# Performance work log

Measured on AMD Instinct MI355X. Metric: run time of the kernel, lower is better.

## Reference

```python
import jax, jax.numpy as jnp
import numpy as np
import hashlib, struct

TABLE_SIZE = 4_194_304
K_DIM = 8
BATCH = 131_072


def _sha_indices(residues_np: np.ndarray, salt: bytes, table_size: int) -> np.ndarray:
    # Faithful to HeritableTrustVault._hash: clamp, *100, int16 bytes, sha256(salt+bytes),
    # little-endian uint64 of first 8 digest bytes, mod table_size.
    q = (np.clip(residues_np, -30000.0, 30000.0) * 100.0).astype(np.int16)
    out = np.empty(q.shape[0], dtype=np.int64)
    for i in range(q.shape[0]):
        d = hashlib.sha256(salt + q[i].tobytes()).digest()
        out[i] = struct.unpack_from('<Q', d)[0] % table_size
    return out


def setup_inputs() -> dict:
    key = jax.random.key(0)
    k0, k1, k2, k3 = jax.random.split(key, 4)
    residues = jax.random.normal(k0, (BATCH, K_DIM), dtype=jnp.float32)
    survivorship = jax.random.uniform(k1, (BATCH,), dtype=jnp.float32)
    trust_table = jax.random.normal(k2, (TABLE_SIZE, K_DIM), dtype=jnp.float32)
    trust_scores = jax.random.uniform(k3, (TABLE_SIZE,), dtype=jnp.float32)
    longevity = jnp.zeros((TABLE_SIZE,), dtype=jnp.int32)
    salt = np.random.RandomState(0).randint(0, 256, 16, dtype=np.uint8).tobytes()
    indices = jnp.asarray(_sha_indices(np.asarray(residues), salt, TABLE_SIZE))
    return {
        'residues': residues,
        'survivorship': survivorship,
        'trust_table': trust_table,
        'trust_scores': trust_scores,
        'longevity': longevity,
        'indices': indices,
    }


def reference(residues, survivorship, trust_table, trust_scores, longevity, indices):
    # update(): serial compare-exchange loop semantics, vectorized.
    # Final score per slot = max(old_score, max survivorship hashing to it).
    # Winner row per slot = FIRST row with survivorship strictly > old score and
    # equal to the final score (strict '>' means later ties never overwrite).
    B = residues.shape[0]
    T = trust_scores.shape[0]
    old_at = trust_scores[indices]                                  # [B]
    new_scores = trust_scores.at[indices].max(survivorship)         # [T]
    final_at = new_scores[indices]                                  # [B]
    win = (survivorship > old_at) & (survivorship >= final_at)      # [B]
    rows = jnp.arange(B, dtype=jnp.int32)
    cand = jnp.where(win, rows, B)                                  # sentinel B = no winner
    min_row = jnp.full((T,), B, dtype=jnp.int32).at[indices].min(cand)
    has_winner = min_row < B                                        # [T]
    safe_row = jnp.where(has_winner, min_row, 0)
    new_table = jnp.where(has_winner[:, None], residues[safe_row], trust_table)
    new_longevity = longevity.at[indices].add(1)
    # query() after update
    query_scores = new_scores[indices]                              # [B]
    return query_scores, new_table, new_scores, new_longevity
```

## Files before the change

kernel.cpp:

```cpp
#include <hip/hip_runtime.h>

#define T_SIZE 4194304
#define B_SIZE 131072
#define KD 8
#define ROW_BLOCKS (B_SIZE / 256)
#define SLOT_BLOCKS (T_SIZE / 256)

typedef unsigned long long u64;
typedef unsigned int u32;

__global__ void vault_init_kernel(const int* __restrict__ longevity,
                                  float* __restrict__ new_longevity,
                                  u64* __restrict__ packed) {
    int t = blockIdx.x * blockDim.x + threadIdx.x;
    ulonglong2 z = {0ull, 0ull};
    ((ulonglong2*)packed)[2 * t]     = z;
    ((ulonglong2*)packed)[2 * t + 1] = z;
    int4 l = ((const int4*)longevity)[t];
    ((float4*)new_longevity)[t] =
        make_float4((float)l.x, (float)l.y, (float)l.z, (float)l.w);
}

__global__ void vault_scatter_kernel(const float* __restrict__ survivorship,
                                     const int* __restrict__ indices,
                                     u64* __restrict__ packed,
                                     float* __restrict__ new_longevity) {
    int i = blockIdx.x * blockDim.x + threadIdx.x;
    int idx = indices[i];
    u32 bits = __float_as_uint(survivorship[i]);
    u64 p = ((u64)bits << 32) | (u64)(~(u32)i);
    atomicMax(packed + idx, p);
    atomicAdd(new_longevity + idx, 1.0f);
}

__global__ void vault_finalize_kernel(const float* __restrict__ residues,
                                      const float* __restrict__ trust_table,
                                      const float* __restrict__ trust_scores,
                                      const int* __restrict__ indices,
                                      const u64* __restrict__ packed,
                                      float* __restrict__ query_scores,
                                      float* __restrict__ new_table,
                                      float* __restrict__ new_scores) {
    int b = blockIdx.x;
    if (b < ROW_BLOCKS) {
        int i = b * 256 + threadIdx.x;
        int idx = indices[i];
        u64 p = packed[idx];
        float ms = __uint_as_float((u32)(p >> 32));
        float oldv = trust_scores[idx];
        query_scores[i] = fmaxf(oldv, ms);
    } else {
        int t = (b - ROW_BLOCKS) * 256 + threadIdx.x;
        u64 p = packed[t];
        float ms = __uint_as_float((u32)(p >> 32));
        float oldv = trust_scores[t];
        new_scores[t] = fmaxf(oldv, ms);
        int r = (int)(~(u32)p);
        const float4* src = (ms > oldv)
            ? (const float4*)(residues + (size_t)r * KD)
            : (const float4*)(trust_table + (size_t)t * KD);
        float4 a = src[0];
        float4 c = src[1];
        float4* dst = (float4*)(new_table + (size_t)t * KD);
        dst[0] = a;
        dst[1] = c;
    }
}

extern "C" void kernel_launch(void* const* d_in, const int* in_sizes, int n_in,
                              void* d_out, int out_size, void* d_ws, size_t ws_size,
                              hipStream_t stream) {
    const float* residues      = (const float*)d_in[0];
    const float* survivorship  = (const float*)d_in[1];
    const float* trust_table   = (const float*)d_in[2];
    const float* trust_scores  = (const float*)d_in[3];
    const int*   longevity     = (const int*)d_in[4];
    const int*   indices       = (const int*)d_in[5];

    float* query_scores  = (float*)d_out;
    float* new_table     = query_scores + B_SIZE;
    float* new_scores    = new_table + (size_t)T_SIZE * KD;
    float* new_longevity = new_scores + T_SIZE;

    u64* packed = (u64*)d_ws;

    const int blk = 256;

    vault_init_kernel<<<T_SIZE / 4 / blk, blk, 0, stream>>>(
        longevity, new_longevity, packed);

    vault_scatter_kernel<<<B_SIZE / blk, blk, 0, stream>>>(
        survivorship, indices, packed, new_longevity);

    vault_finalize_kernel<<<ROW_BLOCKS + SLOT_BLOCKS, blk, 0, stream>>>(
        residues, trust_table, trust_scores, indices, packed,
        query_scores, new_table, new_scores);
}
```

Baseline: 316.3 us.

## Replace dense finalize with bulk copy plus sparse patch of touched slots

Stops zero-initialising the full packed workspace and clears only the slots the indices hit. Replaces the per-slot finalize pass, which read packed state for all 4M slots, with a plain nontemporal streaming copy of the table, scores and longevity, followed by a sparse patch kernel. The patch kernel writes winning rows, updated scores and longevity increments only for touched slots. This cuts read traffic on the packed array, at the cost of an extra launch and scattered writes that must be ordered after the bulk copy.

```diff
diff --git a/kernel.cpp b/kernel.cpp
--- a/kernel.cpp
+++ b/kernel.cpp
@@ -3,65 +3,72 @@
 #define T_SIZE 4194304
 #define B_SIZE 131072
 #define KD 8
-#define ROW_BLOCKS (B_SIZE / 256)
-#define SLOT_BLOCKS (T_SIZE / 256)
+#define TBL_V4 (T_SIZE * KD / 4)
+#define SCR_V4 (T_SIZE / 4)
 
 typedef unsigned long long u64;
 typedef unsigned int u32;
+typedef float f32x4 __attribute__((ext_vector_type(4)));
 
-__global__ void vault_init_kernel(const int* __restrict__ longevity,
-                                  float* __restrict__ new_longevity,
-                                  u64* __restrict__ packed) {
-    int t = blockIdx.x * blockDim.x + threadIdx.x;
-    ulonglong2 z = {0ull, 0ull};
-    ((ulonglong2*)packed)[2 * t]     = z;
-    ((ulonglong2*)packed)[2 * t + 1] = z;
-    int4 l = ((const int4*)longevity)[t];
-    ((float4*)new_longevity)[t] =
-        make_float4((float)l.x, (float)l.y, (float)l.z, (float)l.w);
+__global__ void vault_clear_kernel(const int* __restrict__ indices,
+                                   u64* __restrict__ packed) {
+    int i = blockIdx.x * blockDim.x + threadIdx.x;
+    packed[indices[i]] = 0ull;
 }
 
 __global__ void vault_scatter_kernel(const float* __restrict__ survivorship,
                                      const int* __restrict__ indices,
-                                     u64* __restrict__ packed,
-                                     float* __restrict__ new_longevity) {
+                                     u64* __restrict__ packed) {
     int i = blockIdx.x * blockDim.x + threadIdx.x;
     int idx = indices[i];
     u32 bits = __float_as_uint(survivorship[i]);
     u64 p = ((u64)bits << 32) | (u64)(~(u32)i);
     atomicMax(packed + idx, p);
-    atomicAdd(new_longevity + idx, 1.0f);
 }
 
-__global__ void vault_finalize_kernel(const float* __restrict__ residues,
-                                      const float* __restrict__ trust_table,
-                                      const float* __restrict__ trust_scores,
-                                      const int* __restrict__ indices,
-                                      const u64* __restrict__ packed,
-                                      float* __restrict__ query_scores,
-                                      float* __restrict__ new_table,
-                                      float* __restrict__ new_scores) {
-    int b = blockIdx.x;
-    if (b < ROW_BLOCKS) {
-        int i = b * 256 + threadIdx.x;
-        int idx = indices[i];
-        u64 p = packed[idx];
-        float ms = __uint_as_float((u32)(p >> 32));
-        float oldv = trust_scores[idx];
-        query_scores[i] = fmaxf(oldv, ms);
+__global__ void vault_bulk_kernel(const float* __restrict__ trust_table,
+                                  const float* __restrict__ trust_scores,
+                                  const int* __restrict__ longevity,
+                                  float* __restrict__ new_table,
+                                  float* __restrict__ new_scores,
+                                  float* __restrict__ new_longevity) {
+    int i = blockIdx.x * blockDim.x + threadIdx.x;
+    if (i < TBL_V4) {
+        f32x4 v = __builtin_nontemporal_load((const f32x4*)trust_table + i);
+        __builtin_nontemporal_store(v, (f32x4*)new_table + i);
+    } else if (i < TBL_V4 + SCR_V4) {
+        int j = i - TBL_V4;
+        f32x4 v = __builtin_nontemporal_load((const f32x4*)trust_scores + j);
+        __builtin_nontemporal_store(v, (f32x4*)new_scores + j);
     } else {
-        int t = (b - ROW_BLOCKS) * 256 + threadIdx.x;
-        u64 p = packed[t];
-        float ms = __uint_as_float((u32)(p >> 32));
-        float oldv = trust_scores[t];
-        new_scores[t] = fmaxf(oldv, ms);
-        int r = (int)(~(u32)p);
-        const float4* src = (ms > oldv)
-            ? (const float4*)(residues + (size_t)r * KD)
-            : (const float4*)(trust_table + (size_t)t * KD);
+        int j = i - (TBL_V4 + SCR_V4);
+        int4 l = ((const int4*)longevity)[j];
+        ((float4*)new_longevity)[j] =
+            make_float4((float)l.x, (float)l.y, (float)l.z, (float)l.w);
+    }
+}
+
+__global__ void vault_patch_kernel(const float* __restrict__ residues,
+                                   const float* __restrict__ trust_scores,
+                                   const int* __restrict__ indices,
+                                   const u64* __restrict__ packed,
+                                   float* __restrict__ query_scores,
+                                   float* __restrict__ new_table,
+                                   float* __restrict__ new_scores,
+                                   float* __restrict__ new_longevity) {
+    int i = blockIdx.x * blockDim.x + threadIdx.x;
+    int idx = indices[i];
+    u64 p = packed[idx];
+    float ms = __uint_as_float((u32)(p >> 32));
+    float oldv = trust_scores[idx];
+    query_scores[i] = fmaxf(oldv, ms);
+    atomicAdd(new_longevity + idx, 1.0f);
+    if (ms > oldv && (int)(~(u32)p) == i) {
+        new_scores[idx] = ms;
+        const float4* src = (const float4*)(residues + (size_t)i * KD);
         float4 a = src[0];
         float4 c = src[1];
-        float4* dst = (float4*)(new_table + (size_t)t * KD);
+        float4* dst = (float4*)(new_table + (size_t)idx * KD);
         dst[0] = a;
         dst[1] = c;
     }
@@ -86,13 +93,16 @@
 
     const int blk = 256;
 
-    vault_init_kernel<<<T_SIZE / 4 / blk, blk, 0, stream>>>(
-        longevity, new_longevity, packed);
+    vault_clear_kernel<<<B_SIZE / blk, blk, 0, stream>>>(indices, packed);
 
     vault_scatter_kernel<<<B_SIZE / blk, blk, 0, stream>>>(
-        survivorship, indices, packed, new_longevity);
+        survivorship, indices, packed);
 
-    vault_finalize_kernel<<<ROW_BLOCKS + SLOT_BLOCKS, blk, 0, stream>>>(
-        residues, trust_table, trust_scores, indices, packed,
-        query_scores, new_table, new_scores);
+    vault_bulk_kernel<<<(TBL_V4 + 2 * SCR_V4) / blk, blk, 0, stream>>>(
+        trust_table, trust_scores, longevity,
+        new_table, new_scores, new_longevity);
+
+    vault_patch_kernel<<<B_SIZE / blk, blk, 0, stream>>>(
+        residues, trust_scores, indices, packed,
+        query_scores, new_table, new_scores, new_longevity);
 }
```

Measured after the change: 325.7 us. +3.0%, slower.
